# Optimization experiments

Measured on AMD Instinct MI355X. Metric: run time of the kernel, lower is better.

## Reference

```python
import jax, jax.numpy as jnp
import numpy as np

WS = (4, 4, 4)  # window size
HEADS = 3
HEAD_DIM = 32

def _relative_indices():
    idx = np.array([[x, y, z] for x in range(WS[0]) for y in range(WS[1]) for z in range(WS[2])])
    rel = idx[None, :, :] - idx[:, None, :]  # [T, T, 3]
    rel = rel - rel.min()
    return rel  # values in [0, 2*ws-2]

_REL = _relative_indices()

def setup_inputs() -> dict:
    key = jax.random.key(0)
    k1, k2, k3, k4, k5 = jax.random.split(key, 5)
    dim = 96
    inner = HEADS * HEAD_DIM  # 96
    x = jax.random.normal(k1, (2, 64, 64, 64, dim), dtype=jnp.float32)
    w_qkv = jax.random.normal(k2, (dim, inner * 3), dtype=jnp.float32) * 0.02
    pos_embedding = jax.random.normal(k3, (7, 7, 7), dtype=jnp.float32)
    w_out = jax.random.normal(k4, (inner, dim), dtype=jnp.float32) * 0.02
    b_out = jax.random.normal(k5, (dim,), dtype=jnp.float32) * 0.02
    return {"x": x, "w_qkv": w_qkv, "pos_embedding": pos_embedding,
            "w_out": w_out, "b_out": b_out}

def reference(x, w_qkv, pos_embedding, w_out, b_out):
    b, H, W, D, C = x.shape
    wh, ww, wd = WS
    nwh, nww, nwd = H // wh, W // ww, D // wd
    nw = nwh * nww * nwd
    T = wh * ww * wd  # tokens per window
    scale = HEAD_DIM ** -0.5

    qkv = x @ w_qkv  # [b,H,W,D,3*inner]
    q, k, v = jnp.split(qkv, 3, axis=-1)

    def to_windows(t):
        # [b,H,W,D,h*d] -> [b, h, nw, T, d]
        t = t.reshape(b, nwh, wh, nww, ww, nwd, wd, HEADS, HEAD_DIM)
        t = t.transpose(0, 7, 1, 3, 5, 2, 4, 6, 8)
        return t.reshape(b, HEADS, nw, T, HEAD_DIM)

    q, k, v = map(to_windows, (q, k, v))

    dots = jnp.einsum('bhwid,bhwjd->bhwij', q, k) * scale  # [b,h,nw,T,T]
    bias = pos_embedding[_REL[:, :, 0], _REL[:, :, 1], _REL[:, :, 2]]  # [T,T]
    attn = jax.nn.softmax(dots + bias, axis=-1)
    out = jnp.einsum('bhwij,bhwjd->bhwid', attn, v)  # [b,h,nw,T,d]

    # back to [b,H,W,D,h*d]
    out = out.reshape(b, HEADS, nwh, nww, nwd, wh, ww, wd, HEAD_DIM)
    out = out.transpose(0, 2, 5, 3, 6, 4, 7, 1, 8)
    out = out.reshape(b, H, W, D, HEADS * HEAD_DIM)
    return out @ w_out + b_out
```

## Files before the change

kernel.cpp:

```cpp
#include <hip/hip_runtime.h>


typedef __attribute__((ext_vector_type(8))) short bv8;
typedef __attribute__((ext_vector_type(4))) float fv4;

__device__ __forceinline__ unsigned short f2bf(float f) {
    union { float f; unsigned u; } v; v.f = f;
    unsigned r = v.u + 0x7fffu + ((v.u >> 16) & 1u);
    return (unsigned short)(r >> 16);
}

__device__ __forceinline__ bv8 cvt8(const float* __restrict__ p) {
    float4 a = *(const float4*)p;
    float4 b = *(const float4*)(p + 4);
    bv8 r;
    r[0] = (short)f2bf(a.x); r[1] = (short)f2bf(a.y);
    r[2] = (short)f2bf(a.z); r[3] = (short)f2bf(a.w);
    r[4] = (short)f2bf(b.x); r[5] = (short)f2bf(b.y);
    r[6] = (short)f2bf(b.z); r[7] = (short)f2bf(b.w);
    return r;
}

__global__ void prep_kernel(const float* __restrict__ wqkv,
                            const float* __restrict__ wout,
                            const float* __restrict__ pos,
                            float* __restrict__ bias,
                            unsigned short* __restrict__ wqT,
                            unsigned short* __restrict__ woT)
{
    int id = blockIdx.x * 256 + threadIdx.x;
    if (id < 27648) {
        int n = id / 96, k = id % 96;
        wqT[id] = f2bf(wqkv[k * 288 + n]);
    } else if (id < 36864) {
        int j = id - 27648;
        int n = j / 96, k = j % 96;
        woT[j] = f2bf(wout[k * 96 + n]);
    } else {
        int i = id - 36864;
        int qi = i >> 6, kj = i & 63;
        int dh = ((kj >> 4) & 3) - ((qi >> 4) & 3) + 3;
        int dw = ((kj >> 2) & 3) - ((qi >> 2) & 3) + 3;
        int dd = (kj & 3) - (qi & 3) + 3;
        bias[i] = pos[(dh * 7 + dw) * 7 + dd];
    }
}

__global__ void __launch_bounds__(256, 3) winattn_kernel(
    const float* __restrict__ x,
    const float* __restrict__ b_out,
    const float* __restrict__ bias,
    const unsigned short* __restrict__ wqT,
    const unsigned short* __restrict__ woT,
    float* __restrict__ out)
{
    __shared__ __align__(16) unsigned short qs[64 * 104];
    __shared__ __align__(16) unsigned short ks[64 * 104];
    __shared__ __align__(16) unsigned short vts[96 * 72];
    __shared__ __align__(16) unsigned short ps[4 * 16 * 72];

    const int tid = threadIdx.x;
    const int w = tid >> 6, lane = tid & 63;
    const int c = lane & 15, g = lane >> 4;
    const int widx = blockIdx.x, bb = blockIdx.y;
    const int bh = (widx >> 8) & 15, bw2 = (widx >> 4) & 15, bd = widx & 15;

    const int ST_W = 64 * 96, ST_H = 64 * 64 * 96;
    const int xbase = ((bb * 64 + bh * 4) * 64 + bw2 * 4) * 64 * 96 + bd * 4 * 96;
    const int i0 = w * 16;

    const int mt0 = (w & 1) * 2;
    const int ntbase = (w >> 1) * 9;
    bv8 af[2][3];
#pragma unroll
    for (int m2 = 0; m2 < 2; ++m2) {
        int t = (mt0 + m2) * 16 + c;
        const float* tp = x + xbase + (t >> 4) * ST_H + ((t >> 2) & 3) * ST_W + (t & 3) * 96;
#pragma unroll
        for (int k = 0; k < 3; ++k)
            af[m2][k] = cvt8(tp + k * 32 + g * 8);
    }

    float brow[4][4];
#pragma unroll
    for (int nt = 0; nt < 4; ++nt)
#pragma unroll
        for (int r = 0; r < 4; ++r)
            brow[nt][r] = bias[(i0 + 4 * g + r) * 64 + nt * 16 + c];

    const unsigned short* bsrc = wqT + c * 96 + g * 8;
    bv8 b0[3], bn[3];
#pragma unroll
    for (int k = 0; k < 3; ++k) b0[k] = *(const bv8*)(bsrc + ntbase * 1536 + k * 32);

#pragma unroll
    for (int i = 0; i < 9; ++i) {
        const int nt = ntbase + i;
        if (i < 8) {
#pragma unroll
            for (int k = 0; k < 3; ++k) bn[k] = *(const bv8*)(bsrc + (nt + 1) * 1536 + k * 32);
        }
        fv4 acc0 = {0.f, 0.f, 0.f, 0.f}, acc1 = {0.f, 0.f, 0.f, 0.f};
#pragma unroll
        for (int k = 0; k < 3; ++k) {
            acc0 = __builtin_amdgcn_mfma_f32_16x16x32_bf16(af[0][k], b0[k], acc0, 0, 0, 0);
            acc1 = __builtin_amdgcn_mfma_f32_16x16x32_bf16(af[1][k], b0[k], acc1, 0, 0, 0);
        }
#pragma unroll
        for (int m2 = 0; m2 < 2; ++m2) {
            const fv4& acc = m2 ? acc1 : acc0;
            int row = (mt0 + m2) * 16 + 4 * g;
            if (nt < 6) {
                int col = nt * 16 + c;
#pragma unroll
                for (int r = 0; r < 4; ++r) qs[(row + r) * 104 + col] = f2bf(acc[r]);
            } else if (nt < 12) {
                int col = (nt - 6) * 16 + c;
#pragma unroll
                for (int r = 0; r < 4; ++r) ks[(row + r) * 104 + col] = f2bf(acc[r]);
            } else {
                int d = (nt - 12) * 16 + c;
                unsigned q0 = (unsigned)f2bf(acc[0]) | ((unsigned)f2bf(acc[1]) << 16);
                unsigned q1 = (unsigned)f2bf(acc[2]) | ((unsigned)f2bf(acc[3]) << 16);
                *(unsigned*)&vts[d * 72 + row]     = q0;
                *(unsigned*)&vts[d * 72 + row + 2] = q1;
            }
        }
        if (i < 8) {
#pragma unroll
            for (int k = 0; k < 3; ++k) b0[k] = bn[k];
        }
    }
    __syncthreads();

    const float scale = 0.17677669529663687f;
    unsigned short* pw = ps + w * (16 * 72);

    bv8 qf[3];
#pragma unroll
    for (int h = 0; h < 3; ++h)
        qf[h] = *(const bv8*)&qs[(i0 + c) * 104 + h * 32 + g * 8];

#pragma unroll
    for (int h = 0; h < 3; ++h) {
        bv8 kf[4];
#pragma unroll
        for (int nt = 0; nt < 4; ++nt)
            kf[nt] = *(const bv8*)&ks[(nt * 16 + c) * 104 + h * 32 + g * 8];
        float sv[4][4];
#pragma unroll
        for (int nt = 0; nt < 4; ++nt) {
            fv4 z = {0.f, 0.f, 0.f, 0.f};
            fv4 s = __builtin_amdgcn_mfma_f32_16x16x32_bf16(qf[h], kf[nt], z, 0, 0, 0);
#pragma unroll
            for (int r = 0; r < 4; ++r)
                sv[nt][r] = s[r] * scale + brow[nt][r];
        }
        float mx[4], sm[4];
#pragma unroll
        for (int r = 0; r < 4; ++r)
            mx[r] = fmaxf(fmaxf(sv[0][r], sv[1][r]), fmaxf(sv[2][r], sv[3][r]));
#pragma unroll
        for (int m = 1; m <= 8; m <<= 1)
#pragma unroll
            for (int r = 0; r < 4; ++r)
                mx[r] = fmaxf(mx[r], __shfl_xor(mx[r], m, 64));
#pragma unroll
        for (int r = 0; r < 4; ++r) sm[r] = 0.f;
#pragma unroll
        for (int nt = 0; nt < 4; ++nt)
#pragma unroll
            for (int r = 0; r < 4; ++r) {
                float e = __expf(sv[nt][r] - mx[r]);
                sv[nt][r] = e;
                sm[r] += e;
            }
#pragma unroll
        for (int m = 1; m <= 8; m <<= 1)
#pragma unroll
            for (int r = 0; r < 4; ++r)
                sm[r] += __shfl_xor(sm[r], m, 64);
        float inv[4];
#pragma unroll
        for (int r = 0; r < 4; ++r) inv[r] = __builtin_amdgcn_rcpf(sm[r]);

#pragma unroll
        for (int nt = 0; nt < 4; ++nt)
#pragma unroll
            for (int r = 0; r < 4; ++r)
                pw[(4 * g + r) * 72 + nt * 16 + c] = f2bf(sv[nt][r]);

        bv8 pf[2];
#pragma unroll
        for (int k2 = 0; k2 < 2; ++k2)
            pf[k2] = *(const bv8*)&pw[c * 72 + k2 * 32 + g * 8];

#pragma unroll
        for (int dt = 0; dt < 2; ++dt) {
            fv4 oacc = {0.f, 0.f, 0.f, 0.f};
#pragma unroll
            for (int k2 = 0; k2 < 2; ++k2) {
                bv8 vf = *(const bv8*)&vts[(h * 32 + dt * 16 + c) * 72 + k2 * 32 + g * 8];
                oacc = __builtin_amdgcn_mfma_f32_16x16x32_bf16(pf[k2], vf, oacc, 0, 0, 0);
            }
#pragma unroll
            for (int r = 0; r < 4; ++r)
                qs[(i0 + 4 * g + r) * 104 + h * 32 + dt * 16 + c] = f2bf(oacc[r] * inv[r]);
        }
    }

    bv8 afo[3];
#pragma unroll
    for (int k = 0; k < 3; ++k)
        afo[k] = *(const bv8*)&qs[(i0 + c) * 104 + k * 32 + g * 8];

    const unsigned short* osrc = woT + c * 96 + g * 8;
    bv8 ob0[3], obn[3];
#pragma unroll
    for (int k = 0; k < 3; ++k) ob0[k] = *(const bv8*)(osrc + k * 32);

#pragma unroll
    for (int nt = 0; nt < 6; ++nt) {
        if (nt < 5) {
#pragma unroll
            for (int k = 0; k < 3; ++k) obn[k] = *(const bv8*)(osrc + (nt + 1) * 1536 + k * 32);
        }
        fv4 acc = {0.f, 0.f, 0.f, 0.f};
#pragma unroll
        for (int k = 0; k < 3; ++k)
            acc = __builtin_amdgcn_mfma_f32_16x16x32_bf16(afo[k], ob0[k], acc, 0, 0, 0);
        int cc = nt * 16 + c;
        float bo = b_out[cc];
#pragma unroll
        for (int r = 0; r < 4; ++r) {
            int t = i0 + 4 * g + r;
            out[xbase + (t >> 4) * ST_H + ((t >> 2) & 3) * ST_W + (t & 3) * 96 + cc] = acc[r] + bo;
        }
        if (nt < 5) {
#pragma unroll
            for (int k = 0; k < 3; ++k) ob0[k] = obn[k];
        }
    }
}

extern "C" void kernel_launch(void* const* d_in, const int* in_sizes, int n_in,
                              void* d_out, int out_size, void* d_ws, size_t ws_size,
                              hipStream_t stream)
{
    const float* x    = (const float*)d_in[0];
    const float* wqkv = (const float*)d_in[1];
    const float* pos  = (const float*)d_in[2];
    const float* wout = (const float*)d_in[3];
    const float* bout = (const float*)d_in[4];
    float* out = (float*)d_out;

    float* bias = (float*)d_ws;
    unsigned short* wqT = (unsigned short*)((char*)d_ws + 16384);
    unsigned short* woT = (unsigned short*)((char*)d_ws + 16384 + 55296);

    prep_kernel<<<160, 256, 0, stream>>>(wqkv, wout, pos, bias, wqT, woT);
    winattn_kernel<<<dim3(4096, 2), 256, 0, stream>>>(x, bout, bias, wqT, woT, out);
}
```

Before: 205.9 us.

## Compute transposed scores and pass probabilities through shuffles instead of LDS

Each wave now computes the full QKV projection for its own 16 tokens, which removes the split across waves and the shared Q buffer. The score MFMA is transposed (K times Q), so softmax reductions shrink to two cross-group shuffles. Probabilities are normalized and packed into bf16 pairs, then moved into the PV operand layout with lane shuffles rather than an LDS round trip, and exp2 is used with log2e folded into the scale and bias. The P staging buffer goes away and launch bounds rise to four blocks, trading more shuffle instructions and more projection MFMAs per wave for less LDS traffic and higher occupancy.

```diff
diff --git a/kernel.cpp b/kernel.cpp
--- a/kernel.cpp
+++ b/kernel.cpp
@@ -8,6 +8,10 @@
     union { float f; unsigned u; } v; v.f = f;
     unsigned r = v.u + 0x7fffu + ((v.u >> 16) & 1u);
     return (unsigned short)(r >> 16);
+}
+
+__device__ __forceinline__ unsigned pack2(float lo, float hi) {
+    return (unsigned)f2bf(lo) | ((unsigned)f2bf(hi) << 16);
 }
 
 __device__ __forceinline__ bv8 cvt8(const float* __restrict__ p) {
@@ -24,7 +28,7 @@
 __global__ void prep_kernel(const float* __restrict__ wqkv,
                             const float* __restrict__ wout,
                             const float* __restrict__ pos,
-                            float* __restrict__ bias,
+                            float* __restrict__ biasT,
                             unsigned short* __restrict__ wqT,
                             unsigned short* __restrict__ woT)
 {
@@ -38,26 +42,25 @@
         woT[j] = f2bf(wout[k * 96 + n]);
     } else {
         int i = id - 36864;
-        int qi = i >> 6, kj = i & 63;
+        int kj = i >> 6, qi = i & 63;
         int dh = ((kj >> 4) & 3) - ((qi >> 4) & 3) + 3;
         int dw = ((kj >> 2) & 3) - ((qi >> 2) & 3) + 3;
         int dd = (kj & 3) - (qi & 3) + 3;
-        bias[i] = pos[(dh * 7 + dw) * 7 + dd];
-    }
-}
-
-__global__ void __launch_bounds__(256, 3) winattn_kernel(
+        biasT[kj * 64 + qi] = pos[(dh * 7 + dw) * 7 + dd] * 1.4426950408889634f;
+    }
+}
+
+__global__ void __launch_bounds__(256, 4) winattn_kernel(
     const float* __restrict__ x,
     const float* __restrict__ b_out,
-    const float* __restrict__ bias,
+    const float* __restrict__ biasT,
     const unsigned short* __restrict__ wqT,
     const unsigned short* __restrict__ woT,
     float* __restrict__ out)
 {
-    __shared__ __align__(16) unsigned short qs[64 * 104];
+    __shared__ __align__(16) unsigned short au[4 * 16 * 104];
     __shared__ __align__(16) unsigned short ks[64 * 104];
     __shared__ __align__(16) unsigned short vts[96 * 72];
-    __shared__ __align__(16) unsigned short ps[4 * 16 * 72];
 
     const int tid = threadIdx.x;
     const int w = tid >> 6, lane = tid & 63;
@@ -68,17 +71,15 @@
     const int ST_W = 64 * 96, ST_H = 64 * 64 * 96;
     const int xbase = ((bb * 64 + bh * 4) * 64 + bw2 * 4) * 64 * 96 + bd * 4 * 96;
     const int i0 = w * 16;
-
-    const int mt0 = (w & 1) * 2;
-    const int ntbase = (w >> 1) * 9;
-    bv8 af[2][3];
-#pragma unroll
-    for (int m2 = 0; m2 < 2; ++m2) {
-        int t = (mt0 + m2) * 16 + c;
+    unsigned short* auw = au + w * (16 * 104);
+
+    bv8 af[3];
+    {
+        int t = i0 + c;
         const float* tp = x + xbase + (t >> 4) * ST_H + ((t >> 2) & 3) * ST_W + (t & 3) * 96;
 #pragma unroll
         for (int k = 0; k < 3; ++k)
-            af[m2][k] = cvt8(tp + k * 32 + g * 8);
+            af[k] = cvt8(tp + k * 32 + g * 8);
     }
 
     float brow[4][4];
@@ -86,60 +87,50 @@
     for (int nt = 0; nt < 4; ++nt)
 #pragma unroll
         for (int r = 0; r < 4; ++r)
-            brow[nt][r] = bias[(i0 + 4 * g + r) * 64 + nt * 16 + c];
+            brow[nt][r] = biasT[(nt * 16 + 4 * g + r) * 64 + i0 + c];
 
     const unsigned short* bsrc = wqT + c * 96 + g * 8;
     bv8 b0[3], bn[3];
 #pragma unroll
-    for (int k = 0; k < 3; ++k) b0[k] = *(const bv8*)(bsrc + ntbase * 1536 + k * 32);
-
-#pragma unroll
-    for (int i = 0; i < 9; ++i) {
-        const int nt = ntbase + i;
-        if (i < 8) {
+    for (int k = 0; k < 3; ++k) b0[k] = *(const bv8*)(bsrc + k * 32);
+
+#pragma unroll
+    for (int nt = 0; nt < 18; ++nt) {
+        if (nt < 17) {
 #pragma unroll
             for (int k = 0; k < 3; ++k) bn[k] = *(const bv8*)(bsrc + (nt + 1) * 1536 + k * 32);
         }
-        fv4 acc0 = {0.f, 0.f, 0.f, 0.f}, acc1 = {0.f, 0.f, 0.f, 0.f};
-#pragma unroll
-        for (int k = 0; k < 3; ++k) {
-            acc0 = __builtin_amdgcn_mfma_f32_16x16x32_bf16(af[0][k], b0[k], acc0, 0, 0, 0);
-            acc1 = __builtin_amdgcn_mfma_f32_16x16x32_bf16(af[1][k], b0[k], acc1, 0, 0, 0);
-        }
-#pragma unroll
-        for (int m2 = 0; m2 < 2; ++m2) {
-            const fv4& acc = m2 ? acc1 : acc0;
-            int row = (mt0 + m2) * 16 + 4 * g;
-            if (nt < 6) {
-                int col = nt * 16 + c;
-#pragma unroll
-                for (int r = 0; r < 4; ++r) qs[(row + r) * 104 + col] = f2bf(acc[r]);
-            } else if (nt < 12) {
-                int col = (nt - 6) * 16 + c;
-#pragma unroll
-                for (int r = 0; r < 4; ++r) ks[(row + r) * 104 + col] = f2bf(acc[r]);
-            } else {
-                int d = (nt - 12) * 16 + c;
-                unsigned q0 = (unsigned)f2bf(acc[0]) | ((unsigned)f2bf(acc[1]) << 16);
-                unsigned q1 = (unsigned)f2bf(acc[2]) | ((unsigned)f2bf(acc[3]) << 16);
-                *(unsigned*)&vts[d * 72 + row]     = q0;
-                *(unsigned*)&vts[d * 72 + row + 2] = q1;
-            }
-        }
-        if (i < 8) {
-#pragma unroll
-            for (int k = 0; k < 3; ++k) b0[k] = bn[k];
-        }
+        fv4 acc = {0.f, 0.f, 0.f, 0.f};
+#pragma unroll
+        for (int k = 0; k < 3; ++k)
+            acc = __builtin_amdgcn_mfma_f32_16x16x32_bf16(af[k], b0[k], acc, 0, 0, 0);
+        if (nt < 6) {
+#pragma unroll
+            for (int r = 0; r < 4; ++r)
+                auw[(4 * g + r) * 104 + nt * 16 + c] = f2bf(acc[r]);
+        } else if (nt < 12) {
+#pragma unroll
+            for (int r = 0; r < 4; ++r)
+                ks[(i0 + 4 * g + r) * 104 + (nt - 6) * 16 + c] = f2bf(acc[r]);
+        } else {
+            int d = (nt - 12) * 16 + c;
+            *(unsigned*)&vts[d * 72 + i0 + 4 * g]     = pack2(acc[0], acc[1]);
+            *(unsigned*)&vts[d * 72 + i0 + 4 * g + 2] = pack2(acc[2], acc[3]);
+        }
+#pragma unroll
+        for (int k = 0; k < 3; ++k) b0[k] = bn[k];
     }
     __syncthreads();
 
-    const float scale = 0.17677669529663687f;
-    unsigned short* pw = ps + w * (16 * 72);
-
     bv8 qf[3];
 #pragma unroll
     for (int h = 0; h < 3; ++h)
-        qf[h] = *(const bv8*)&qs[(i0 + c) * 104 + h * 32 + g * 8];
+        qf[h] = *(const bv8*)&auw[c * 104 + h * 32 + g * 8];
+
+    const float scale2 = 0.17677669529663687f * 1.4426950408889634f;
+    const int lsrc0 = (((2 * g) & 3) << 4) + c;
+    const int lsrc1 = (((2 * g + 1) & 3) << 4) + c;
+    const bool selhi = (g & 2) != 0;
 
 #pragma unroll
     for (int h = 0; h < 3; ++h) {
@@ -151,50 +142,59 @@
 #pragma unroll
         for (int nt = 0; nt < 4; ++nt) {
             fv4 z = {0.f, 0.f, 0.f, 0.f};
-            fv4 s = __builtin_amdgcn_mfma_f32_16x16x32_bf16(qf[h], kf[nt], z, 0, 0, 0);
-#pragma unroll
-            for (int r = 0; r < 4; ++r)
-                sv[nt][r] = s[r] * scale + brow[nt][r];
-        }
-        float mx[4], sm[4];
-#pragma unroll
-        for (int r = 0; r < 4; ++r)
-            mx[r] = fmaxf(fmaxf(sv[0][r], sv[1][r]), fmaxf(sv[2][r], sv[3][r]));
-#pragma unroll
-        for (int m = 1; m <= 8; m <<= 1)
-#pragma unroll
-            for (int r = 0; r < 4; ++r)
-                mx[r] = fmaxf(mx[r], __shfl_xor(mx[r], m, 64));
-#pragma unroll
-        for (int r = 0; r < 4; ++r) sm[r] = 0.f;
+            fv4 s = __builtin_amdgcn_mfma_f32_16x16x32_bf16(kf[nt], qf[h], z, 0, 0, 0);
+#pragma unroll
+            for (int r = 0; r < 4; ++r)
+                sv[nt][r] = s[r] * scale2 + brow[nt][r];
+        }
+        float m01 = fmaxf(fmaxf(sv[0][0], sv[0][1]), fmaxf(sv[0][2], sv[0][3]));
+        float m11 = fmaxf(fmaxf(sv[1][0], sv[1][1]), fmaxf(sv[1][2], sv[1][3]));
+        float m21 = fmaxf(fmaxf(sv[2][0], sv[2][1]), fmaxf(sv[2][2], sv[2][3]));
+        float m31 = fmaxf(fmaxf(sv[3][0], sv[3][1]), fmaxf(sv[3][2], sv[3][3]));
+        float mx = fmaxf(fmaxf(m01, m11), fmaxf(m21, m31));
+        mx = fmaxf(mx, __shfl_xor(mx, 16, 64));
+        mx = fmaxf(mx, __shfl_xor(mx, 32, 64));
+        float sm = 0.f;
 #pragma unroll
         for (int nt = 0; nt < 4; ++nt)
 #pragma unroll
             for (int r = 0; r < 4; ++r) {
-                float e = __expf(sv[nt][r] - mx[r]);
+                float e = exp2f(sv[nt][r] - mx);
                 sv[nt][r] = e;
-                sm[r] += e;
+                sm += e;
             }
-#pragma unroll
-        for (int m = 1; m <= 8; m <<= 1)
-#pragma unroll
-            for (int r = 0; r < 4; ++r)
-                sm[r] += __shfl_xor(sm[r], m, 64);
-        float inv[4];
-#pragma unroll
-        for (int r = 0; r < 4; ++r) inv[r] = __builtin_amdgcn_rcpf(sm[r]);
-
-#pragma unroll
-        for (int nt = 0; nt < 4; ++nt)
-#pragma unroll
-            for (int r = 0; r < 4; ++r)
-                pw[(4 * g + r) * 72 + nt * 16 + c] = f2bf(sv[nt][r]);
-
+        sm += __shfl_xor(sm, 16, 64);
+        sm += __shfl_xor(sm, 32, 64);
+        float inv = __builtin_amdgcn_rcpf(sm);
+
+        unsigned pk[4][2];
+#pragma unroll
+        for (int nt = 0; nt < 4; ++nt) {
+            pk[nt][0] = pack2(sv[nt][0] * inv, sv[nt][1] * inv);
+            pk[nt][1] = pack2(sv[nt][2] * inv, sv[nt][3] * inv);
+        }
         bv8 pf[2];
 #pragma unroll
-        for (int k2 = 0; k2 < 2; ++k2)
-            pf[k2] = *(const bv8*)&pw[c * 72 + k2 * 32 + g * 8];
-
+        for (int k2 = 0; k2 < 2; ++k2) {
+            unsigned w0 = (unsigned)__shfl((int)pk[2 * k2][0],     lsrc0, 64);
+            unsigned w1 = (unsigned)__shfl((int)pk[2 * k2][1],     lsrc0, 64);
+            unsigned w2 = (unsigned)__shfl((int)pk[2 * k2][0],     lsrc1, 64);
+            unsigned w3 = (unsigned)__shfl((int)pk[2 * k2][1],     lsrc1, 64);
+            unsigned v0 = (unsigned)__shfl((int)pk[2 * k2 + 1][0], lsrc0, 64);
+            unsigned v1 = (unsigned)__shfl((int)pk[2 * k2 + 1][1], lsrc0, 64);
+            unsigned v2 = (unsigned)__shfl((int)pk[2 * k2 + 1][0], lsrc1, 64);
+            unsigned v3 = (unsigned)__shfl((int)pk[2 * k2 + 1][1], lsrc1, 64);
+            unsigned u0 = selhi ? v0 : w0;
+            unsigned u1 = selhi ? v1 : w1;
+            unsigned u2 = selhi ? v2 : w2;
+            unsigned u3 = selhi ? v3 : w3;
+            bv8 p;
+            p[0] = (short)(u0 & 0xffffu); p[1] = (short)(u0 >> 16);
+            p[2] = (short)(u1 & 0xffffu); p[3] = (short)(u1 >> 16);
+            p[4] = (short)(u2 & 0xffffu); p[5] = (short)(u2 >> 16);
+            p[6] = (short)(u3 & 0xffffu); p[7] = (short)(u3 >> 16);
+            pf[k2] = p;
+        }
 #pragma unroll
         for (int dt = 0; dt < 2; ++dt) {
             fv4 oacc = {0.f, 0.f, 0.f, 0.f};
@@ -205,14 +205,14 @@
             }
 #pragma unroll
             for (int r = 0; r < 4; ++r)
-                qs[(i0 + 4 * g + r) * 104 + h * 32 + dt * 16 + c] = f2bf(oacc[r] * inv[r]);
+                auw[(4 * g + r) * 104 + h * 32 + dt * 16 + c] = f2bf(oacc[r]);
         }
     }
 
     bv8 afo[3];
 #pragma unroll
     for (int k = 0; k < 3; ++k)
-        afo[k] = *(const bv8*)&qs[(i0 + c) * 104 + k * 32 + g * 8];
+        afo[k] = *(const bv8*)&auw[c * 104 + k * 32 + g * 8];
 
     const unsigned short* osrc = woT + c * 96 + g * 8;
     bv8 ob0[3], obn[3];
@@ -236,10 +236,8 @@
             int t = i0 + 4 * g + r;
             out[xbase + (t >> 4) * ST_H + ((t >> 2) & 3) * ST_W + (t & 3) * 96 + cc] = acc[r] + bo;
         }
-        if (nt < 5) {
-#pragma unroll
-            for (int k = 0; k < 3; ++k) ob0[k] = obn[k];
-        }
+#pragma unroll
+        for (int k = 0; k < 3; ++k) ob0[k] = obn[k];
     }
 }
 
@@ -254,10 +252,10 @@
     const float* bout = (const float*)d_in[4];
     float* out = (float*)d_out;
 
-    float* bias = (float*)d_ws;
+    float* biasT = (float*)d_ws;
     unsigned short* wqT = (unsigned short*)((char*)d_ws + 16384);
     unsigned short* woT = (unsigned short*)((char*)d_ws + 16384 + 55296);
 
-    prep_kernel<<<160, 256, 0, stream>>>(wqkv, wout, pos, bias, wqT, woT);
-    winattn_kernel<<<dim3(4096, 2), 256, 0, stream>>>(x, bout, bias, wqT, woT, out);
-}
+    prep_kernel<<<160, 256, 0, stream>>>(wqkv, wout, pos, biasT, wqT, woT);
+    winattn_kernel<<<dim3(4096, 2), 256, 0, stream>>>(x, bout, biasT, wqT, woT, out);
+}
```

Result: no change. 205.2 us (-0.4%).
